# Kernel tuning notes

Measured on AMD Instinct MI355X. Metric: run time of the kernel, lower is better.

## Reference

```python
import jax, jax.numpy as jnp
import numpy as np

H = 768
NH = 12
HD = 64
R = 4
SCALING = 8.0 / 4.0  # lora_alpha / r


def setup_inputs() -> dict:
    key = jax.random.key(0)
    ks = jax.random.split(key, 16)
    B, T = 16, 512
    s = 0.02
    x = jax.random.normal(ks[0], (B, T, H), dtype=jnp.float32)
    mask = jax.random.randint(ks[1], (B, T), 0, 2, dtype=jnp.int32)
    return {
        "x": x,
        "mask": mask,
        "Wq": jax.random.normal(ks[2], (H, H), jnp.float32) * s,
        "bq": jnp.zeros((H,), jnp.float32),
        "Aq": jax.random.normal(ks[3], (R, H), jnp.float32) * s,
        "Bq": jax.random.normal(ks[4], (H, R), jnp.float32) * s,
        "Wk": jax.random.normal(ks[5], (H, H), jnp.float32) * s,
        "bk": jnp.zeros((H,), jnp.float32),
        "Wv": jax.random.normal(ks[6], (H, H), jnp.float32) * s,
        "bv": jnp.zeros((H,), jnp.float32),
        "Av": jax.random.normal(ks[7], (R, H), jnp.float32) * s,
        "Bv": jax.random.normal(ks[8], (H, R), jnp.float32) * s,
        "Wo": jax.random.normal(ks[9], (H, H), jnp.float32) * s,
        "bo": jnp.zeros((H,), jnp.float32),
    }


def _lora_linear(x, W, b, A, Bm):
    # base: x @ W^T + b ; lora: (x @ A^T) @ B^T * scaling (dropout inactive at eval)
    return x @ W.T + b + (x @ A.T) @ Bm.T * SCALING


def reference(x, mask, Wq, bq, Aq, Bq, Wk, bk, Wv, bv, Av, Bv, Wo, bo):
    B, T, _ = x.shape
    q = _lora_linear(x, Wq, bq, Aq, Bq).reshape(B, T, NH, HD).transpose(0, 2, 1, 3)
    k = (x @ Wk.T + bk).reshape(B, T, NH, HD).transpose(0, 2, 1, 3)
    v = _lora_linear(x, Wv, bv, Av, Bv).reshape(B, T, NH, HD).transpose(0, 2, 1, 3)
    # [B, NH, T, T]
    scores = jnp.einsum("bhqd,bhkd->bhqk", q, k) / jnp.sqrt(jnp.float32(HD))
    m = (mask == 0)[:, None, None, :]  # mask key positions where mask==0
    scores = jnp.where(m, jnp.float32(-1e9), scores)
    attn = jax.nn.softmax(scores, axis=-1)  # dropout inactive at eval
    out = jnp.einsum("bhqk,bhkd->bhqd", attn, v)
    out = out.transpose(0, 2, 1, 3).reshape(B, T, H)
    return out @ Wo.T + bo
```

## Files before the change

### kernel.cpp

```cpp
#include <hip/hip_runtime.h>
#include <stdint.h>

#define H 768
#define NHEAD 12
#define HDIM 64
#define BATCH 16
#define TSEQ 512
#define BT (BATCH*TSEQ)
#define C3 (3*H)
#define LDQK 1536

typedef __attribute__((ext_vector_type(8))) short short8;
typedef __attribute__((ext_vector_type(4))) float floatx4;
typedef unsigned short u16;

__device__ __forceinline__ u16 f2bf(float f) {
    union { float f; unsigned int u; } v; v.f = f;
    unsigned int u = v.u;
    return (u16)((u + 0x7FFFu + ((u >> 16) & 1u)) >> 16);
}

__device__ __forceinline__ void async_ld16(const void* g, void* l) {
    __builtin_amdgcn_global_load_lds((__attribute__((address_space(1))) void*)g,
                                     (__attribute__((address_space(3))) void*)l,
                                     16, 0, 0);
}

#define PREP_BLOCKS 9216
#define CVT_BLOCKS  6144
__global__ void prep_kernel(const float* __restrict__ Wq, const float* __restrict__ bq,
                            const float* __restrict__ Aq, const float* __restrict__ Bq,
                            const float* __restrict__ Wk, const float* __restrict__ bk,
                            const float* __restrict__ Wv, const float* __restrict__ bv,
                            const float* __restrict__ Av, const float* __restrict__ Bv,
                            const float* __restrict__ Wo, const float* __restrict__ x,
                            u16* __restrict__ Wall, u16* __restrict__ Wobf,
                            float* __restrict__ bias_all, u16* __restrict__ xb)
{
    const int bid = blockIdx.x;
    if (bid >= PREP_BLOCKS) {
        const int i = ((bid - PREP_BLOCKS) * 256 + threadIdx.x) * 4;
        const float4 v = *(const float4*)(x + i);
        u16 o[4] = { f2bf(v.x), f2bf(v.y), f2bf(v.z), f2bf(v.w) };
        *(uint2*)(xb + i) = *(const uint2*)o;
        return;
    }
    const int idx = bid * 256 + threadIdx.x;
    const int r = idx / H;
    const int c = idx - r * H;
    if (r < H) {
        float v = Wq[idx] + 2.0f * (Bq[r*4+0]*Aq[c] + Bq[r*4+1]*Aq[H+c] +
                                    Bq[r*4+2]*Aq[2*H+c] + Bq[r*4+3]*Aq[3*H+c]);
        Wall[idx] = f2bf(v);
    } else if (r < 2*H) {
        Wall[idx] = f2bf(Wk[idx - H*H]);
    } else if (r < 3*H) {
        const int rr = r - 2*H;
        float v = Wv[rr*H + c] + 2.0f * (Bv[rr*4+0]*Av[c] + Bv[rr*4+1]*Av[H+c] +
                                         Bv[rr*4+2]*Av[2*H+c] + Bv[rr*4+3]*Av[3*H+c]);
        Wall[idx] = f2bf(v);
    } else {
        Wobf[idx - 3*H*H] = f2bf(Wo[idx - 3*H*H]);
    }
    if (idx < C3) {
        bias_all[idx] = (idx < H) ? bq[idx] : (idx < 2*H ? bk[idx - H] : bv[idx - 2*H]);
    }
}

template<int MODE, int TM>
__global__ __launch_bounds__(256)
void gemm_bt(const u16* __restrict__ A, const u16* __restrict__ Bw,
             const float* __restrict__ bias, void* __restrict__ Cout,
             u16* __restrict__ Vout, int K, int ldc)
{
    constexpr int MT = TM / 32;
    __shared__ u16 Ablk[TM * 32];
    __shared__ u16 Bblk[128 * 32];
    const int tid  = threadIdx.x;
    const int wave = tid >> 6;
    const int lane = tid & 63;
    const int quad = lane >> 4;
    const int l16  = lane & 15;
    const int m0 = blockIdx.y * TM;
    const int n0 = blockIdx.x * 128;
    const int mw = (wave & 1) * (TM / 2);
    const int nw = (wave >> 1) * 64;

    const int srow = lane >> 2;
    const int scol = (lane & 3) * 8;
    const int arow0 = wave * (TM / 4);
    const u16* gA = A  + (size_t)(m0 + arow0 + srow) * K + scol;
    const u16* gB = Bw + (size_t)(n0 + wave*32 + srow) * K + scol;
    u16* lA = Ablk + arow0 * 32;
    u16* lB = Bblk + wave * 32 * 32;

    floatx4 acc[MT][4] = {};

    for (int k0 = 0; k0 < K; k0 += 32) {
        __syncthreads();
        async_ld16(gA + k0, lA);
        if (TM == 128) async_ld16(gA + k0 + 16*K, lA + 16*32);
        async_ld16(gB + k0, lB);
        async_ld16(gB + k0 + 16*K, lB + 16*32);
        __syncthreads();
        short8 af[MT], bfr[4];
        #pragma unroll
        for (int mt = 0; mt < MT; mt++)
            af[mt] = *(const short8*)(Ablk + (mw + mt*16 + l16)*32 + quad*8);
        #pragma unroll
        for (int nt = 0; nt < 4; nt++)
            bfr[nt] = *(const short8*)(Bblk + (nw + nt*16 + l16)*32 + quad*8);
        #pragma unroll
        for (int mt = 0; mt < MT; mt++)
            #pragma unroll
            for (int nt = 0; nt < 4; nt++)
                acc[mt][nt] = __builtin_amdgcn_mfma_f32_16x16x32_bf16(af[mt], bfr[nt], acc[mt][nt], 0, 0, 0);
    }

    if (MODE == 1 && n0 >= LDQK) {
        const int nv = n0 + nw - LDQK;
        const int b  = m0 >> 9;
        #pragma unroll
        for (int nt = 0; nt < 4; nt++) {
            const int n  = nv + nt*16 + l16;
            const int hh = n >> 6, d = n & 63;
            const float bv = bias[LDQK + n];
            u16* vp = Vout + ((size_t)(b*NHEAD + hh) * HDIM + d) * TSEQ;
            #pragma unroll
            for (int mt = 0; mt < MT; mt++) {
                const int t0 = (m0 & 511) + mw + mt*16 + quad*4;
                u16 pack[4];
                #pragma unroll
                for (int r = 0; r < 4; r++) pack[r] = f2bf(acc[mt][nt][r] + bv);
                *(uint2*)(vp + t0) = *(const uint2*)pack;
            }
        }
    } else {
        #pragma unroll
        for (int nt = 0; nt < 4; nt++) {
            const int n = n0 + nw + nt*16 + l16;
            const float bv = bias[n];
            #pragma unroll
            for (int mt = 0; mt < MT; mt++) {
                #pragma unroll
                for (int r = 0; r < 4; r++) {
                    const int m = m0 + mw + mt*16 + quad*4 + r;
                    const float v = acc[mt][nt][r] + bv;
                    if (MODE == 1) ((u16*)Cout)[(size_t)m * ldc + n] = f2bf(v);
                    else           ((float*)Cout)[(size_t)m * ldc + n] = v;
                }
            }
        }
    }
}

#define PSTRIDE 40

__global__ __launch_bounds__(256)
void attn_kernel(const u16* __restrict__ qk, const u16* __restrict__ vt,
                 const int* __restrict__ mask, u16* __restrict__ attn_out)
{
    __shared__ float maskadd[TSEQ];
    __shared__ u16 Kbuf[2][32 * 64];
    __shared__ u16 Vbuf[2][64 * 32];
    __shared__ u16 Pbuf[4][2][16 * PSTRIDE];

    const int qt = blockIdx.x;
    const int bh = blockIdx.y;
    const int b = bh / NHEAD, h = bh - b * NHEAD;
    const int tid  = threadIdx.x;
    const int wave = tid >> 6;
    const int lane = tid & 63;
    const int quad = lane >> 4;
    const int l16  = lane & 15;

    for (int i = tid; i < TSEQ; i += 256)
        maskadd[i] = (mask[b*TSEQ + i] == 0) ? -1e9f : 0.0f;

    const size_t btok = (size_t)b * TSEQ;
    const int q0 = qt * 128 + wave * 32;

    short8 qf[2][2];
    #pragma unroll
    for (int m = 0; m < 2; m++) {
        const u16* qp = qk + (btok + q0 + m*16 + l16) * LDQK + h*HDIM + quad*8;
        qf[m][0] = *(const short8*)qp;
        qf[m][1] = *(const short8*)(qp + 32);
    }

    const u16* kglob = qk + btok * LDQK + H + h*HDIM;
    const u16* vglob = vt + (size_t)bh * HDIM * TSEQ;

    auto stage = [&](int kb, int pp) {
        {
            const int r = lane >> 3;
            const int g = (lane & 7) ^ r;
            async_ld16(kglob + (size_t)(kb + wave*8 + r) * LDQK + g*8,
                       &Kbuf[pp][wave*8*64]);
        }
        {
            const int dr = lane >> 2;
            const int g  = (lane & 3) ^ ((dr >> 1) & 3);
            async_ld16(vglob + (size_t)(wave*16 + dr) * TSEQ + kb + g*8,
                       &Vbuf[pp][wave*16*32]);
        }
    };

    floatx4 o[2][4] = {};
    float lsum[2][4] = {};

    auto compute = [&](int kb, int pp) {
        const u16* Kb_ = Kbuf[pp];
        const u16* Vb_ = Vbuf[pp];
        short8 kf[2][2];
        #pragma unroll
        for (int t = 0; t < 2; t++)
            #pragma unroll
            for (int h2 = 0; h2 < 2; h2++)
                kf[t][h2] = *(const short8*)(Kb_ + (t*16 + l16)*64 + (((h2*4 + quad) ^ (l16 & 7))*8));
        short8 vf[4];
        #pragma unroll
        for (int dt = 0; dt < 4; dt++)
            vf[dt] = *(const short8*)(Vb_ + (dt*16 + l16)*32 + ((quad ^ ((l16 >> 1) & 3))*8));

        floatx4 s[2][2];
        #pragma unroll
        for (int m = 0; m < 2; m++)
            #pragma unroll
            for (int t = 0; t < 2; t++) {
                floatx4 acc = {0.f, 0.f, 0.f, 0.f};
                acc = __builtin_amdgcn_mfma_f32_16x16x32_bf16(qf[m][0], kf[t][0], acc, 0, 0, 0);
                acc = __builtin_amdgcn_mfma_f32_16x16x32_bf16(qf[m][1], kf[t][1], acc, 0, 0, 0);
                s[m][t] = acc;
            }
        const float m0 = maskadd[kb + l16];
        const float m1 = maskadd[kb + 16 + l16];
        #pragma unroll
        for (int m = 0; m < 2; m++) {
            u16* Pw = Pbuf[wave][m];
            #pragma unroll
            for (int r = 0; r < 4; r++) {
                const float p0 = __expf(s[m][0][r] * 0.125f + m0);
                const float p1 = __expf(s[m][1][r] * 0.125f + m1);
                lsum[m][r] += p0 + p1;
                Pw[(quad*4 + r) * PSTRIDE + l16]      = f2bf(p0);
                Pw[(quad*4 + r) * PSTRIDE + 16 + l16] = f2bf(p1);
            }
        }
        #pragma unroll
        for (int m = 0; m < 2; m++) {
            const short8 pa = *(const short8*)(Pbuf[wave][m] + l16 * PSTRIDE + quad*8);
            #pragma unroll
            for (int dt = 0; dt < 4; dt++)
                o[m][dt] = __builtin_amdgcn_mfma_f32_16x16x32_bf16(pa, vf[dt], o[m][dt], 0, 0, 0);
        }
    };

    stage(0, 0);
    for (int it = 0; it < 16; it++) {
        __syncthreads();
        if (it < 15) stage((it + 1) * 32, (it + 1) & 1);
        compute(it * 32, it & 1);
    }

    #pragma unroll
    for (int m = 0; m < 2; m++) {
        float inv[4];
        #pragma unroll
        for (int r = 0; r < 4; r++) {
            float l = lsum[m][r];
            l += __shfl_xor(l, 1);
            l += __shfl_xor(l, 2);
            l += __shfl_xor(l, 4);
            l += __shfl_xor(l, 8);
            inv[r] = 1.0f / l;
        }
        #pragma unroll
        for (int dt = 0; dt < 4; dt++)
            #pragma unroll
            for (int r = 0; r < 4; r++) {
                const int q = q0 + m*16 + quad*4 + r;
                attn_out[(btok + q) * H + h*HDIM + dt*16 + l16] = f2bf(o[m][dt][r] * inv[r]);
            }
    }
}

extern "C" void kernel_launch(void* const* d_in, const int* in_sizes, int n_in,
                              void* d_out, int out_size, void* d_ws, size_t ws_size,
                              hipStream_t stream)
{
    const float* x   = (const float*)d_in[0];
    const int* mask  = (const int*)d_in[1];
    const float* Wq  = (const float*)d_in[2];
    const float* bq  = (const float*)d_in[3];
    const float* Aq  = (const float*)d_in[4];
    const float* Bq  = (const float*)d_in[5];
    const float* Wk  = (const float*)d_in[6];
    const float* bk  = (const float*)d_in[7];
    const float* Wv  = (const float*)d_in[8];
    const float* bv  = (const float*)d_in[9];
    const float* Av  = (const float*)d_in[10];
    const float* Bv  = (const float*)d_in[11];
    const float* Wo  = (const float*)d_in[12];
    const float* bo  = (const float*)d_in[13];

    char* ws = (char*)d_ws;
    u16*   xb      = (u16*)  (ws);
    u16*   Wall    = (u16*)  (ws + 12582912);
    u16*   Wobf    = (u16*)  (ws + 16121856);
    float* biasall = (float*)(ws + 17301504);
    u16*   qk      = (u16*)  (ws + 17310720);
    u16*   vt      = (u16*)  (ws + 42476544);
    u16*   attn_o  = (u16*)  (ws + 55059456);

    prep_kernel<<<PREP_BLOCKS + CVT_BLOCKS, 256, 0, stream>>>(
        Wq, bq, Aq, Bq, Wk, bk, Wv, bv, Av, Bv, Wo, x, Wall, Wobf, biasall, xb);
    gemm_bt<1,128><<<dim3(C3/128, BT/128), 256, 0, stream>>>(xb, Wall, biasall, qk, vt, H, LDQK);
    attn_kernel<<<dim3(TSEQ/128, BATCH*NHEAD), 256, 0, stream>>>(qk, vt, mask, attn_o);
    gemm_bt<0,64><<<dim3(H/128, BT/64), 256, 0, stream>>>(attn_o, Wobf, bo, d_out, nullptr, H, H);
}
```

Before: 223.6 us.

## Double GEMM K-tile with XOR-swizzled LDS, move V transpose to separate kernel

```diff
diff --git a/kernel.cpp b/kernel.cpp
--- a/kernel.cpp
+++ b/kernel.cpp
@@ -8,7 +8,6 @@
 #define TSEQ 512
 #define BT (BATCH*TSEQ)
 #define C3 (3*H)
-#define LDQK 1536
 
 typedef __attribute__((ext_vector_type(8))) short short8;
 typedef __attribute__((ext_vector_type(4))) float floatx4;
@@ -71,11 +70,11 @@
 __global__ __launch_bounds__(256)
 void gemm_bt(const u16* __restrict__ A, const u16* __restrict__ Bw,
              const float* __restrict__ bias, void* __restrict__ Cout,
-             u16* __restrict__ Vout, int K, int ldc)
+             int K, int ldc)
 {
     constexpr int MT = TM / 32;
-    __shared__ u16 Ablk[TM * 32];
-    __shared__ u16 Bblk[128 * 32];
+    __shared__ u16 Ablk[TM * 64];
+    __shared__ u16 Bblk[128 * 64];
     const int tid  = threadIdx.x;
     const int wave = tid >> 6;
     const int lane = tid & 63;
@@ -86,78 +85,95 @@
     const int mw = (wave & 1) * (TM / 2);
     const int nw = (wave >> 1) * 64;
 
-    const int srow = lane >> 2;
-    const int scol = (lane & 3) * 8;
-    const int arow0 = wave * (TM / 4);
-    const u16* gA = A  + (size_t)(m0 + arow0 + srow) * K + scol;
-    const u16* gB = Bw + (size_t)(n0 + wave*32 + srow) * K + scol;
-    u16* lA = Ablk + arow0 * 32;
-    u16* lB = Bblk + wave * 32 * 32;
+    const int r8 = lane >> 3;
+    const int kgs = ((lane & 7) ^ r8) * 8;
+    const u16* gA = A  + (size_t)(m0 + wave*(TM/4) + r8) * K + kgs;
+    const u16* gB = Bw + (size_t)(n0 + wave*32      + r8) * K + kgs;
+    u16* lA = Ablk + wave * (TM/4) * 64;
+    u16* lB = Bblk + wave * 32 * 64;
 
     floatx4 acc[MT][4] = {};
-
-    for (int k0 = 0; k0 < K; k0 += 32) {
+    const int sw = l16 & 7;
+
+    for (int k0 = 0; k0 < K; k0 += 64) {
         __syncthreads();
-        async_ld16(gA + k0, lA);
-        if (TM == 128) async_ld16(gA + k0 + 16*K, lA + 16*32);
-        async_ld16(gB + k0, lB);
-        async_ld16(gB + k0 + 16*K, lB + 16*32);
+        #pragma unroll
+        for (int j = 0; j < TM/32; j++)
+            async_ld16(gA + k0 + (size_t)(j*8) * K, lA + j*8*64);
+        #pragma unroll
+        for (int j = 0; j < 4; j++)
+            async_ld16(gB + k0 + (size_t)(j*8) * K, lB + j*8*64);
         __syncthreads();
-        short8 af[MT], bfr[4];
-        #pragma unroll
-        for (int mt = 0; mt < MT; mt++)
-            af[mt] = *(const short8*)(Ablk + (mw + mt*16 + l16)*32 + quad*8);
-        #pragma unroll
-        for (int nt = 0; nt < 4; nt++)
-            bfr[nt] = *(const short8*)(Bblk + (nw + nt*16 + l16)*32 + quad*8);
-        #pragma unroll
-        for (int mt = 0; mt < MT; mt++)
+        #pragma unroll
+        for (int kk = 0; kk < 2; kk++) {
+            short8 af[MT], bfr[4];
+            #pragma unroll
+            for (int mt = 0; mt < MT; mt++)
+                af[mt] = *(const short8*)(Ablk + (mw + mt*16 + l16)*64 + ((quad + 4*kk) ^ sw)*8);
             #pragma unroll
             for (int nt = 0; nt < 4; nt++)
-                acc[mt][nt] = __builtin_amdgcn_mfma_f32_16x16x32_bf16(af[mt], bfr[nt], acc[mt][nt], 0, 0, 0);
-    }
-
-    if (MODE == 1 && n0 >= LDQK) {
-        const int nv = n0 + nw - LDQK;
-        const int b  = m0 >> 9;
-        #pragma unroll
-        for (int nt = 0; nt < 4; nt++) {
-            const int n  = nv + nt*16 + l16;
-            const int hh = n >> 6, d = n & 63;
-            const float bv = bias[LDQK + n];
-            u16* vp = Vout + ((size_t)(b*NHEAD + hh) * HDIM + d) * TSEQ;
-            #pragma unroll
-            for (int mt = 0; mt < MT; mt++) {
-                const int t0 = (m0 & 511) + mw + mt*16 + quad*4;
-                u16 pack[4];
+                bfr[nt] = *(const short8*)(Bblk + (nw + nt*16 + l16)*64 + ((quad + 4*kk) ^ sw)*8);
+            #pragma unroll
+            for (int mt = 0; mt < MT; mt++)
                 #pragma unroll
-                for (int r = 0; r < 4; r++) pack[r] = f2bf(acc[mt][nt][r] + bv);
-                *(uint2*)(vp + t0) = *(const uint2*)pack;
+                for (int nt = 0; nt < 4; nt++)
+                    acc[mt][nt] = __builtin_amdgcn_mfma_f32_16x16x32_bf16(af[mt], bfr[nt], acc[mt][nt], 0, 0, 0);
+        }
+    }
+
+    #pragma unroll
+    for (int nt = 0; nt < 4; nt++) {
+        const int n = n0 + nw + nt*16 + l16;
+        const float bv = bias[n];
+        #pragma unroll
+        for (int mt = 0; mt < MT; mt++) {
+            #pragma unroll
+            for (int r = 0; r < 4; r++) {
+                const int m = m0 + mw + mt*16 + quad*4 + r;
+                const float v = acc[mt][nt][r] + bv;
+                if (MODE == 1) ((u16*)Cout)[(size_t)m * ldc + n] = f2bf(v);
+                else           ((float*)Cout)[(size_t)m * ldc + n] = v;
             }
         }
-    } else {
-        #pragma unroll
-        for (int nt = 0; nt < 4; nt++) {
-            const int n = n0 + nw + nt*16 + l16;
-            const float bv = bias[n];
-            #pragma unroll
-            for (int mt = 0; mt < MT; mt++) {
-                #pragma unroll
-                for (int r = 0; r < 4; r++) {
-                    const int m = m0 + mw + mt*16 + quad*4 + r;
-                    const float v = acc[mt][nt][r] + bv;
-                    if (MODE == 1) ((u16*)Cout)[(size_t)m * ldc + n] = f2bf(v);
-                    else           ((float*)Cout)[(size_t)m * ldc + n] = v;
-                }
-            }
-        }
+    }
+}
+
+#define TSTRIDE 72
+__global__ __launch_bounds__(256)
+void vtrans_kernel(const u16* __restrict__ qkv, u16* __restrict__ vt)
+{
+    __shared__ u16 Lt[64 * TSTRIDE];
+    const int tc = blockIdx.x;
+    const int bh = blockIdx.y;
+    const int b = bh / NHEAD, h = bh - b * NHEAD;
+    const int tid = threadIdx.x;
+
+    {
+        const int tok = tid & 63;
+        const int dg  = (tid >> 6) * 16;
+        const u16* p = qkv + (size_t)(b*TSEQ + tc*64 + tok) * C3 + 2*H + h*HDIM + dg;
+        u16 tmp[16];
+        *(short8*)tmp       = *(const short8*)p;
+        *(short8*)(tmp + 8) = *(const short8*)(p + 8);
+        #pragma unroll
+        for (int j = 0; j < 16; j++) Lt[(dg + j) * TSTRIDE + tok] = tmp[j];
+    }
+    __syncthreads();
+    {
+        const int d  = tid >> 2;
+        const int ts = (tid & 3) * 16;
+        uint4 a0 = *(const uint4*)(Lt + d * TSTRIDE + ts);
+        uint4 a1 = *(const uint4*)(Lt + d * TSTRIDE + ts + 8);
+        u16* op = vt + ((size_t)bh * HDIM + d) * TSEQ + tc*64 + ts;
+        *(uint4*)op       = a0;
+        *(uint4*)(op + 8) = a1;
     }
 }
 
 #define PSTRIDE 40
 
 __global__ __launch_bounds__(256)
-void attn_kernel(const u16* __restrict__ qk, const u16* __restrict__ vt,
+void attn_kernel(const u16* __restrict__ qkv, const u16* __restrict__ vt,
                  const int* __restrict__ mask, u16* __restrict__ attn_out)
 {
     __shared__ float maskadd[TSEQ];
@@ -183,19 +199,19 @@
     short8 qf[2][2];
     #pragma unroll
     for (int m = 0; m < 2; m++) {
-        const u16* qp = qk + (btok + q0 + m*16 + l16) * LDQK + h*HDIM + quad*8;
+        const u16* qp = qkv + (btok + q0 + m*16 + l16) * C3 + h*HDIM + quad*8;
         qf[m][0] = *(const short8*)qp;
         qf[m][1] = *(const short8*)(qp + 32);
     }
 
-    const u16* kglob = qk + btok * LDQK + H + h*HDIM;
+    const u16* kglob = qkv + btok * C3 + H + h*HDIM;
     const u16* vglob = vt + (size_t)bh * HDIM * TSEQ;
 
     auto stage = [&](int kb, int pp) {
         {
             const int r = lane >> 3;
             const int g = (lane & 7) ^ r;
-            async_ld16(kglob + (size_t)(kb + wave*8 + r) * LDQK + g*8,
+            async_ld16(kglob + (size_t)(kb + wave*8 + r) * C3 + g*8,
                        &Kbuf[pp][wave*8*64]);
         }
         {
@@ -309,13 +325,14 @@
     u16*   Wall    = (u16*)  (ws + 12582912);
     u16*   Wobf    = (u16*)  (ws + 16121856);
     float* biasall = (float*)(ws + 17301504);
-    u16*   qk      = (u16*)  (ws + 17310720);
-    u16*   vt      = (u16*)  (ws + 42476544);
+    u16*   qkv     = (u16*)  (ws + 17310720);
     u16*   attn_o  = (u16*)  (ws + 55059456);
+    u16*   vt      = xb;
 
     prep_kernel<<<PREP_BLOCKS + CVT_BLOCKS, 256, 0, stream>>>(
         Wq, bq, Aq, Bq, Wk, bk, Wv, bv, Av, Bv, Wo, x, Wall, Wobf, biasall, xb);
-    gemm_bt<1,128><<<dim3(C3/128, BT/128), 256, 0, stream>>>(xb, Wall, biasall, qk, vt, H, LDQK);
-    attn_kernel<<<dim3(TSEQ/128, BATCH*NHEAD), 256, 0, stream>>>(qk, vt, mask, attn_o);
-    gemm_bt<0,64><<<dim3(H/128, BT/64), 256, 0, stream>>>(attn_o, Wobf, bo, d_out, nullptr, H, H);
-}
+    gemm_bt<1,128><<<dim3(C3/128, BT/128), 256, 0, stream>>>(xb, Wall, biasall, qkv, H, C3);
+    vtrans_kernel<<<dim3(TSEQ/64, BATCH*NHEAD), 256, 0, stream>>>(qkv, vt);
+    attn_kernel<<<dim3(TSEQ/128, BATCH*NHEAD), 256, 0, stream>>>(qkv, vt, mask, attn_o);
+    gemm_bt<0,64><<<dim3(H/128, BT/64), 256, 0, stream>>>(attn_o, Wobf, bo, d_out, H, H);
+}
```

Result: faster. 214.1 us (-4.3%).
